# Kernel tuning notes

Hardware: AMD Instinct MI355X
Metric: run time of the kernel (lower is better)

The kernel has to match this reference:

```python
import jax, jax.numpy as jnp
import numpy as np

B, L, D_MODEL, D_K, HEADS, C = 4, 4096, 512, 64, 8, 2
TOPK = int(C * np.log(L))  # int(c * log(input_seq_len)) = 16


def setup_inputs() -> dict:
    key = jax.random.key(0)
    ks = jax.random.split(key, 5)
    q_in = jax.random.normal(ks[0], (B, L, D_MODEL), jnp.float32)
    k_in = jax.random.normal(ks[1], (B, L, D_MODEL), jnp.float32)
    v_in = jax.random.normal(ks[2], (B, L, D_MODEL), jnp.float32)
    Wq = jax.random.normal(ks[3], (D_MODEL, D_K), jnp.float32) / np.sqrt(D_MODEL)
    bq = jax.random.normal(ks[4], (D_K,), jnp.float32) * 0.01
    return {"q_in": q_in, "k_in": k_in, "v_in": v_in, "Wq": Wq, "bq": bq}


def _to_heads(x, Wq, bq):
    # Faithful to original: ALL of q/k/v use the `query` Dense layer, and all
    # heads are identical copies (same projection stacked `heads` times).
    p = x @ Wq + bq                       # [B, L, d_k]
    p = jnp.swapaxes(p, 1, 2)             # [B, d_k, L]  (transpose [0,3,2,1] of [B,L,d,H])
    return jnp.broadcast_to(p[:, None], (p.shape[0], HEADS, D_K, p.shape[-1]))  # [B,H,d,L]


def reference(q_in, k_in, v_in, Wq, bq):
    Q = jnp.fft.fft(_to_heads(q_in, Wq, bq).astype(jnp.complex64), axis=-1)
    K = jnp.fft.fft(_to_heads(k_in, Wq, bq).astype(jnp.complex64), axis=-1)
    V = _to_heads(v_in, Wq, bq)           # [B,H,d,L] float32
    QK = jnp.fft.ifft(Q * jnp.conj(K), axis=-1)   # circular cross-correlation
    qk_abs = jnp.abs(QK)                  # [B,H,d,L]

    vals, idx = jax.lax.top_k(qk_abs, TOPK)       # [B,H,d,k]
    w = jax.nn.softmax(vals, axis=-1)             # softmax over the k lags

    # tf.roll(v, shift=-lag): out[t] = v[(t + lag) mod L]  -> vectorized gather
    t = jnp.arange(L, dtype=jnp.int32)
    gidx = (idx[..., None] + t) % L               # [B,H,d,k,L]
    Vk = jnp.broadcast_to(V[:, :, :, None, :], gidx.shape)
    rolled = jnp.take_along_axis(Vk, gidx, axis=-1)           # [B,H,d,k,L]
    agg = jnp.sum(rolled * w[..., None], axis=3)              # [B,H,d,L]

    out = agg.reshape(agg.shape[0], HEADS * D_K, L)           # [B, H*d, L]
    return jnp.transpose(out, (0, 2, 1))                      # [B, L, H*d]
```

## Files before the change

### kernel.cpp

```cpp
#include <hip/hip_runtime.h>
#include <hip/hip_bf16.h>

#define BQ 4
#define LQ 4096
#define DM 512
#define DK 64
#define NROWS (BQ * DK)
#define TOPK 16
#define CAND 32

typedef __attribute__((ext_vector_type(4))) short short4v;
typedef __attribute__((ext_vector_type(8))) short short8v;
typedef __attribute__((ext_vector_type(16))) float f32x16;

__device__ __forceinline__ unsigned short f2bf(float x) {
  unsigned u = __builtin_bit_cast(unsigned, x);
  return (unsigned short)((u + 0x7FFFu + ((u >> 16) & 1u)) >> 16);
}
__device__ __forceinline__ float bf2f(unsigned short h) {
  unsigned u = ((unsigned)h) << 16;
  return __builtin_bit_cast(float, u);
}

__global__ __launch_bounds__(256) void proj_kernel(
    const float* __restrict__ q_in, const float* __restrict__ k_in,
    const float* __restrict__ v_in, const float* __restrict__ Wq,
    const float* __restrict__ bq, float* __restrict__ ws) {
  const float* x = blockIdx.z == 0 ? q_in : (blockIdx.z == 1 ? k_in : v_in);
  float* outp = ws + (size_t)blockIdx.z * (size_t)(NROWS * LQ);

  __shared__ __align__(16) short sm[27648];
  short* xh = sm;
  short* xl = sm + 9216;
  short* wh = sm + 18432;
  short* wl = sm + 23040;

  const int tid = threadIdx.x;
  const int l = tid & 63, wv = tid >> 6;
  const int R0 = blockIdx.x * 128;

  const int srow = tid >> 1;
  const int sp0 = (tid & 1) * 8;
  const int wcol = tid & 63;
  const int wk0 = (tid >> 6) * 16;

  f32x16 acc[2];
#pragma unroll
  for (int nt = 0; nt < 2; ++nt)
#pragma unroll
    for (int i = 0; i < 16; ++i) acc[nt][i] = 0.f;

  float4 xr[8];
  float wr[16];
#pragma unroll
  for (int c = 0; c < 8; ++c)
    xr[c] = *reinterpret_cast<const float4*>(
        &x[(size_t)(R0 + srow) * DM + (sp0 + c) * 4]);
#pragma unroll
  for (int u = 0; u < 16; ++u)
    wr[u] = Wq[(size_t)(wk0 + u) * DK + wcol];

  const int arow = wv * 32 + (l & 31);
  const int qn = l >> 5;
  const int aswz = 2 * ((arow >> 3) & 3);
  const int bc0 = l & 31;
  const int bswz0 = 2 * (((0 + bc0) >> 3) & 3);
  const int bswz1 = 2 * (((32 + bc0) >> 3) & 3);

  for (int kc = 0; kc < DM; kc += 64) {
    __syncthreads();
#pragma unroll
    for (int c = 0; c < 8; ++c) {
      int f4 = sp0 + c;
      int qd = (f4 >> 1) ^ (2 * ((srow >> 3) & 3));
      int base = srow * 72 + qd * 8 + (f4 & 1) * 4;
      float vv[4] = {xr[c].x, xr[c].y, xr[c].z, xr[c].w};
      short4v hi, lo;
#pragma unroll
      for (int i = 0; i < 4; ++i) {
        unsigned short h = f2bf(vv[i]);
        hi[i] = (short)h;
        lo[i] = (short)f2bf(vv[i] - bf2f(h));
      }
      *reinterpret_cast<short4v*>(xh + base) = hi;
      *reinterpret_cast<short4v*>(xl + base) = lo;
    }
#pragma unroll
    for (int qq = 0; qq < 2; ++qq) {
      int qd = ((wk0 >> 3) + qq) ^ (2 * ((wcol >> 3) & 3));
      int base = wcol * 72 + qd * 8;
      short8v hi, lo;
#pragma unroll
      for (int i = 0; i < 8; ++i) {
        float vv = wr[qq * 8 + i];
        unsigned short h = f2bf(vv);
        hi[i] = (short)h;
        lo[i] = (short)f2bf(vv - bf2f(h));
      }
      *reinterpret_cast<short8v*>(wh + base) = hi;
      *reinterpret_cast<short8v*>(wl + base) = lo;
    }
    __syncthreads();
    if (kc + 64 < DM) {
#pragma unroll
      for (int c = 0; c < 8; ++c)
        xr[c] = *reinterpret_cast<const float4*>(
            &x[(size_t)(R0 + srow) * DM + kc + 64 + (sp0 + c) * 4]);
#pragma unroll
      for (int u = 0; u < 16; ++u)
        wr[u] = Wq[(size_t)(kc + 64 + wk0 + u) * DK + wcol];
    }
#pragma unroll
    for (int ks = 0; ks < 4; ++ks) {
      int qA = (2 * ks + qn) ^ aswz;
      short8v ah = *reinterpret_cast<const short8v*>(xh + arow * 72 + qA * 8);
      short8v al_ = *reinterpret_cast<const short8v*>(xl + arow * 72 + qA * 8);
      {
        int qB = (2 * ks + qn) ^ bswz0;
        short8v bh = *reinterpret_cast<const short8v*>(wh + bc0 * 72 + qB * 8);
        short8v bl_ = *reinterpret_cast<const short8v*>(wl + bc0 * 72 + qB * 8);
        asm volatile("v_mfma_f32_32x32x16_bf16 %0, %1, %2, %0"
                     : "+v"(acc[0]) : "v"(ah), "v"(bh));
        asm volatile("v_mfma_f32_32x32x16_bf16 %0, %1, %2, %0"
                     : "+v"(acc[0]) : "v"(ah), "v"(bl_));
        asm volatile("v_mfma_f32_32x32x16_bf16 %0, %1, %2, %0"
                     : "+v"(acc[0]) : "v"(al_), "v"(bh));
      }
      {
        int qB = (2 * ks + qn) ^ bswz1;
        short8v bh = *reinterpret_cast<const short8v*>(wh + (32 + bc0) * 72 + qB * 8);
        short8v bl_ = *reinterpret_cast<const short8v*>(wl + (32 + bc0) * 72 + qB * 8);
        asm volatile("v_mfma_f32_32x32x16_bf16 %0, %1, %2, %0"
                     : "+v"(acc[1]) : "v"(ah), "v"(bh));
        asm volatile("v_mfma_f32_32x32x16_bf16 %0, %1, %2, %0"
                     : "+v"(acc[1]) : "v"(ah), "v"(bl_));
        asm volatile("v_mfma_f32_32x32x16_bf16 %0, %1, %2, %0"
                     : "+v"(acc[1]) : "v"(al_), "v"(bh));
      }
    }
  }

  asm volatile("s_nop 7\n\ts_nop 7\n\ts_nop 7" ::: "memory");
  __syncthreads();
  float* ts = (float*)sm;
  const int b = R0 >> 12, i0 = R0 & (LQ - 1);
  float bb[2] = {bq[l & 31], bq[32 + (l & 31)]};
#pragma unroll
  for (int nt = 0; nt < 2; ++nt) {
    float* area = ts + (wv * 2 + nt) * 1088;
#pragma unroll
    for (int r = 0; r < 16; ++r) {
      int io = (r & 3) + 8 * (r >> 2) + 4 * (l >> 5);
      area[(l & 31) * 34 + io] = acc[nt][r] + bb[nt];
    }
  }
  __syncthreads();
  const int e = l & 15, jg = l >> 4;
#pragma unroll
  for (int nt = 0; nt < 2; ++nt) {
    const float* area = ts + (wv * 2 + nt) * 1088;
#pragma unroll
    for (int p = 0; p < 8; ++p) {
      int jj = jg * 8 + p;
      float2 v = *reinterpret_cast<const float2*>(area + jj * 34 + e * 2);
      *reinterpret_cast<float2*>(
          &outp[((size_t)b * DK + nt * 32 + jj) * LQ + i0 + wv * 32 + e * 2]) = v;
    }
  }
}

__global__ __launch_bounds__(512) void corr_topk_kernel(
    const float* __restrict__ qp, const float* __restrict__ kp,
    float* __restrict__ lw) {
  const int row = blockIdx.x;
  const int tid = threadIdx.x;
  __shared__ __align__(16) short qs[3 * 4112 + 4096];
  __shared__ __align__(16) short ks[4096];
  __shared__ __align__(16) float qf[LQ];
  __shared__ __align__(16) float kf[LQ];
  __shared__ unsigned wk[128];
  __shared__ unsigned scand[CAND];
  __shared__ float rS[CAND];
  __shared__ float ordv[TOPK]; __shared__ int ordl[TOPK];

  const float* qr = qp + ((size_t)row << 12);
  const float* kr = kp + ((size_t)row << 12);

  {
    const float4* q4 = (const float4*)qr;
    float4 v0 = q4[tid * 2], v1 = q4[tid * 2 + 1];
    float4 v2 = q4[(tid * 2 + 2) & 1023];
    ((float4*)qf)[tid * 2] = v0;
    ((float4*)qf)[tid * 2 + 1] = v1;
    float f[12] = {v0.x, v0.y, v0.z, v0.w, v1.x, v1.y, v1.z, v1.w,
                   v2.x, v2.y, v2.z, v2.w};
#pragma unroll
    for (int r = 0; r < 4; ++r) {
      short8v o;
#pragma unroll
      for (int i = 0; i < 8; ++i) o[i] = (short)f2bf(f[i + r]);
      *(short8v*)(&qs[r * 4112 + tid * 8]) = o;
    }
    const float4* k4 = (const float4*)kr;
    float4 w0 = k4[tid * 2], w1 = k4[tid * 2 + 1];
    ((float4*)kf)[tid * 2] = w0;
    ((float4*)kf)[tid * 2 + 1] = w1;
    float g[8] = {w0.x, w0.y, w0.z, w0.w, w1.x, w1.y, w1.z, w1.w};
    int Q = tid;
    int Qs = Q ^ ((Q >> 3) & 7);
    short8v o;
#pragma unroll
    for (int i = 0; i < 8; ++i) o[i] = (short)f2bf(g[i]);
    *(short8v*)(&ks[Qs << 3]) = o;
  }
  __syncthreads();

  const int l = tid & 63, wv = tid >> 6;
  const int Oq = ((8 * (l >> 5) - 32 * (l & 31)) & 4095) >> 3;
  const int rB = (l & 31) & 3;
  const int Ce = (l & 31) + 8 * (l >> 5) - rB;
  const short* qb = qs + rB * 4112;

  f32x16 acc[4];
#pragma unroll
  for (int M = 0; M < 4; ++M)
#pragma unroll
    for (int i = 0; i < 16; ++i) acc[M][i] = 0.f;

  const int J0 = wv * 32;
#pragma unroll 2
  for (int jb = 0; jb < 32; ++jb) {
    const int J = J0 + jb;
    int e1 = (Ce + 16 * J) & 4095;
    int e2 = (e1 + 4) & 4095;
    uint2 blo = *(const uint2*)(qb + e1);
    uint2 bhi = *(const uint2*)(qb + e2);
    int4 bi; bi.x = blo.x; bi.y = blo.y; bi.z = bhi.x; bi.w = bhi.y;
    short8v bf = __builtin_bit_cast(short8v, bi);
    const int Dq = 2 * J;
#pragma unroll
    for (int M = 0; M < 4; ++M) {
      int Q = (Oq + Dq - 128 * M) & 511;
      Q ^= (Q >> 3) & 7;
      short8v af = *(const short8v*)(&ks[Q << 3]);
      asm volatile("v_mfma_f32_32x32x16_bf16 %0, %1, %2, %0"
                   : "+v"(acc[M]) : "v"(af), "v"(bf));
    }
  }

  asm volatile("s_nop 7\n\ts_nop 7\n\ts_nop 7" ::: "memory");
  __syncthreads();
  float* red = (float*)qs;
  const int strip = (wv & 1) * 4096;
  const int ch4 = (l >> 5) * 4, cn = l & 31;
#define RIDX(M, r) (strip + ((M) << 10) + 32 * (((r)&3) + 8 * ((r) >> 2) + ch4) + cn)
  if (wv < 2) {
#pragma unroll
    for (int M = 0; M < 4; ++M)
#pragma unroll
      for (int r = 0; r < 16; ++r) red[RIDX(M, r)] = acc[M][r];
  }
  __syncthreads();
  if (wv >= 2 && wv < 4) {
#pragma unroll
    for (int M = 0; M < 4; ++M)
#pragma unroll
      for (int r = 0; r < 16; ++r) red[RIDX(M, r)] += acc[M][r];
  }
  __syncthreads();
  if (wv >= 4 && wv < 6) {
#pragma unroll
    for (int M = 0; M < 4; ++M)
#pragma unroll
      for (int r = 0; r < 16; ++r) red[RIDX(M, r)] += acc[M][r];
  }
  __syncthreads();
  if (wv >= 6) {
#pragma unroll
    for (int M = 0; M < 4; ++M)
#pragma unroll
      for (int r = 0; r < 16; ++r) red[RIDX(M, r)] += acc[M][r];
  }
  __syncthreads();
#undef RIDX

  {
    unsigned key[8];
#pragma unroll
    for (int i = 0; i < 8; ++i) {
      int tau = wv * 512 + i * 64 + l;
      float v = red[tau] + red[4096 + tau];
      unsigned u = __builtin_bit_cast(unsigned, fabsf(v));
      key[i] = (u & 0xFFFFF000u) | (unsigned)(4095 - tau);
    }
    unsigned bkey = key[0];
#pragma unroll
    for (int i = 1; i < 8; ++i) bkey = key[i] > bkey ? key[i] : bkey;
    for (int round = 0; round < 16; ++round) {
      unsigned m = bkey;
#pragma unroll
      for (int off = 1; off < 64; off <<= 1) {
        unsigned o = __shfl_xor(m, off);
        m = o > m ? o : m;
      }
      if (l == 0) wk[wv * 16 + round] = m;
#pragma unroll
      for (int i = 0; i < 8; ++i) key[i] = (key[i] == m) ? 0u : key[i];
      bkey = key[0];
#pragma unroll
      for (int i = 1; i < 8; ++i) bkey = key[i] > bkey ? key[i] : bkey;
    }
  }
  __syncthreads();

  if (tid < 128) {
    unsigned ki = wk[tid];
    int rank = 0;
    for (int j = 0; j < 128; ++j) rank += (wk[j] > ki);
    if (rank < CAND) scand[rank] = ki;
  }
  __syncthreads();

  {
    const int ci = tid >> 4, sub = tid & 15;
    const int lag = 4095 - (int)(scand[ci] & 0xFFFu);
    float S0 = 0.f, S1 = 0.f, S2 = 0.f, S3 = 0.f;
    for (int it = 0; it < 256; it += 4) {
      int t0 = (it + 0) * 16 + sub, t1 = (it + 1) * 16 + sub;
      int t2 = (it + 2) * 16 + sub, t3 = (it + 3) * 16 + sub;
      S0 = fmaf(kf[t0], qf[(t0 + lag) & 4095], S0);
      S1 = fmaf(kf[t1], qf[(t1 + lag) & 4095], S1);
      S2 = fmaf(kf[t2], qf[(t2 + lag) & 4095], S2);
      S3 = fmaf(kf[t3], qf[(t3 + lag) & 4095], S3);
    }
    float S = (S0 + S1) + (S2 + S3);
    S += __shfl_xor(S, 1);
    S += __shfl_xor(S, 2);
    S += __shfl_xor(S, 4);
    S += __shfl_xor(S, 8);
    if (sub == 0) rS[ci] = S;
  }
  __syncthreads();

  if (tid < CAND) {
    float vi = fabsf(rS[tid]);
    int ii = 4095 - (int)(scand[tid] & 0xFFFu);
    int rank = 0;
    for (int j = 0; j < CAND; ++j) {
      float vj = fabsf(rS[j]);
      int ij = 4095 - (int)(scand[j] & 0xFFFu);
      rank += (vj > vi) || (vj == vi && ij < ii);
    }
    if (rank < TOPK) { ordv[rank] = vi; ordl[rank] = ii; }
  }
  __syncthreads();

  if (tid == 0) {
    float m0 = ordv[0], s = 0.f, e[TOPK];
    for (int k = 0; k < TOPK; ++k) { e[k] = expf(ordv[k] - m0); s += e[k]; }
    float inv = 1.f / s;
    int* ip = (int*)(lw + (size_t)row * 32);
    for (int k = 0; k < TOPK; ++k) {
      ip[k] = ordl[k];
      ((float*)ip)[TOPK + k] = e[k] * inv;
    }
  }
}

__global__ void agg_kernel(const float* __restrict__ vpT,
                           const float* __restrict__ lw,
                           float* __restrict__ aggT) {
  const int row = blockIdx.x, tid = threadIdx.x;
  __shared__ __align__(16) float vr[2 * LQ];
  __shared__ float w[TOPK]; __shared__ int lg[TOPK];

  const float* v0 = vpT + (size_t)row * LQ;
  for (int x = tid; x < LQ; x += 256) {
    float val = v0[x];
    vr[x] = val; vr[x + LQ] = val;
  }
  if (tid < TOPK) {
    lg[tid] = ((const int*)(lw + (size_t)row * 32))[tid];
    w[tid] = lw[(size_t)row * 32 + TOPK + tid];
  }
  __syncthreads();

  float wr[TOPK]; int lr[TOPK];
#pragma unroll
  for (int k = 0; k < TOPK; ++k) { wr[k] = w[k]; lr[k] = lg[k]; }

  for (int m = 0; m < 16; ++m) {
    int t = m * 256 + tid;
    float a = 0.f;
#pragma unroll
    for (int k = 0; k < TOPK; ++k) a = fmaf(wr[k], vr[t + lr[k]], a);
    aggT[(size_t)row * LQ + t] = a;
  }
}

__global__ void trans_kernel(const float* __restrict__ aggT,
                             float* __restrict__ out) {
  const int b = blockIdx.y;
  const int t0 = blockIdx.x * 64;
  const int tid = threadIdx.x;
  __shared__ float ts[64][65];

#pragma unroll
  for (int v = 0; v < 16; ++v) {
    int f = v * 256 + tid;
    int d = f >> 6, tt = f & 63;
    ts[d][tt] = aggT[((size_t)b * DK + d) * LQ + t0 + tt];
  }
  __syncthreads();

#pragma unroll
  for (int v = 0; v < 128; ++v) {
    int f = v * 256 + tid;
    int tt = f >> 9, c = f & 511;
    out[((size_t)b * LQ + t0 + tt) * (8 * DK) + c] = ts[c & 63][tt];
  }
}

extern "C" void kernel_launch(void* const* d_in, const int* in_sizes, int n_in,
                              void* d_out, int out_size, void* d_ws, size_t ws_size,
                              hipStream_t stream) {
  const float* q_in = (const float*)d_in[0];
  const float* k_in = (const float*)d_in[1];
  const float* v_in = (const float*)d_in[2];
  const float* Wq   = (const float*)d_in[3];
  const float* bq   = (const float*)d_in[4];
  float* out = (float*)d_out;
  float* ws  = (float*)d_ws;

  const size_t M = (size_t)NROWS * LQ;
  float* qp   = ws;
  float* kp   = ws + M;
  float* vp   = ws + 2 * M;
  float* lw   = ws + 3 * M;
  float* aggT = ws + 4 * M;

  proj_kernel<<<dim3(128, 1, 3), 256, 0, stream>>>(q_in, k_in, v_in, Wq, bq, ws);
  corr_topk_kernel<<<NROWS, 512, 0, stream>>>(qp, kp, lw);
  agg_kernel<<<NROWS, 256, 0, stream>>>(vp, lw, aggT);
  trans_kernel<<<dim3(LQ / 64, BQ), 256, 0, stream>>>(aggT, out);
}
```

Measured before the change: 76.48 us.

## Precompute split-bf16 transposed weights and stream projection operands directly into registers

A new small kernel converts Wq once per call into transposed bf16 hi/lo arrays in the workspace. The projection kernel then gives each wave its own 32 rows and loads the A fragments from global memory straight into registers, double-buffered, with B fragments read from the pre-split weights. This removes the LDS staging, the swizzling and the per-chunk __syncthreads. In exchange it adds an extra kernel launch and explicit s_nop padding around the MFMA instructions in both kernels, which may stall the instruction stream in the correlation kernel.

```diff
diff --git a/kernel.cpp b/kernel.cpp
--- a/kernel.cpp
+++ b/kernel.cpp
@@ -9,7 +9,6 @@
 #define TOPK 16
 #define CAND 32
 
-typedef __attribute__((ext_vector_type(4))) short short4v;
 typedef __attribute__((ext_vector_type(8))) short short8v;
 typedef __attribute__((ext_vector_type(16))) float f32x16;
 
@@ -22,27 +21,62 @@
   return __builtin_bit_cast(float, u);
 }
 
+__device__ __forceinline__ void mfma_drain() {
+  __builtin_amdgcn_sched_barrier(0);
+  asm volatile("s_nop 7\n\ts_nop 7\n\ts_nop 7\n\ts_nop 7" ::: "memory");
+  __builtin_amdgcn_sched_barrier(0);
+}
+
+__global__ __launch_bounds__(256) void wprep_kernel(
+    const float* __restrict__ Wq, short* __restrict__ whT,
+    short* __restrict__ wlT) {
+  __shared__ short lh[64][66];
+  __shared__ short ll[64][66];
+  const int tid = threadIdx.x;
+  const int k0 = blockIdx.x * 64;
+#pragma unroll
+  for (int p = 0; p < 16; ++p) {
+    int idx = p * 256 + tid;
+    int kr = idx >> 6, j = idx & 63;
+    float v = Wq[(size_t)(k0 + kr) * DK + j];
+    unsigned short h = f2bf(v);
+    lh[j][kr] = (short)h;
+    ll[j][kr] = (short)f2bf(v - bf2f(h));
+  }
+  __syncthreads();
+  const int j = tid >> 2, ks = (tid & 3) * 16;
+  short8v o0, o1;
+#pragma unroll
+  for (int i = 0; i < 8; ++i) { o0[i] = lh[j][ks + i]; o1[i] = lh[j][ks + 8 + i]; }
+  *(short8v*)(&whT[(size_t)j * DM + k0 + ks]) = o0;
+  *(short8v*)(&whT[(size_t)j * DM + k0 + ks + 8]) = o1;
+#pragma unroll
+  for (int i = 0; i < 8; ++i) { o0[i] = ll[j][ks + i]; o1[i] = ll[j][ks + 8 + i]; }
+  *(short8v*)(&wlT[(size_t)j * DM + k0 + ks]) = o0;
+  *(short8v*)(&wlT[(size_t)j * DM + k0 + ks + 8]) = o1;
+}
+
 __global__ __launch_bounds__(256) void proj_kernel(
     const float* __restrict__ q_in, const float* __restrict__ k_in,
-    const float* __restrict__ v_in, const float* __restrict__ Wq,
-    const float* __restrict__ bq, float* __restrict__ ws) {
+    const float* __restrict__ v_in, const short* __restrict__ whT,
+    const short* __restrict__ wlT, const float* __restrict__ bq,
+    float* __restrict__ ws) {
   const float* x = blockIdx.z == 0 ? q_in : (blockIdx.z == 1 ? k_in : v_in);
   float* outp = ws + (size_t)blockIdx.z * (size_t)(NROWS * LQ);
 
-  __shared__ __align__(16) short sm[27648];
-  short* xh = sm;
-  short* xl = sm + 9216;
-  short* wh = sm + 18432;
-  short* wl = sm + 23040;
+  __shared__ __align__(16) float ts[8 * 1088];
 
   const int tid = threadIdx.x;
   const int l = tid & 63, wv = tid >> 6;
-  const int R0 = blockIdx.x * 128;
-
-  const int srow = tid >> 1;
-  const int sp0 = (tid & 1) * 8;
-  const int wcol = tid & 63;
-  const int wk0 = (tid >> 6) * 16;
+  const int gw = blockIdx.x * 4 + wv;
+  const int R0 = gw * 32;
+  const int koff = 8 * (l >> 5);
+
+  const float* xb = x + (size_t)(R0 + (l & 31)) * DM + koff;
+  const short* bh0p = whT + (size_t)(l & 31) * DM + koff;
+  const short* bl0p = wlT + (size_t)(l & 31) * DM + koff;
+  const short* bh1p = whT + (size_t)(32 + (l & 31)) * DM + koff;
+  const short* bl1p = wlT + (size_t)(32 + (l & 31)) * DM + koff;
 
   f32x16 acc[2];
 #pragma unroll
@@ -50,99 +84,59 @@
 #pragma unroll
     for (int i = 0; i < 16; ++i) acc[nt][i] = 0.f;
 
-  float4 xr[8];
-  float wr[16];
-#pragma unroll
-  for (int c = 0; c < 8; ++c)
-    xr[c] = *reinterpret_cast<const float4*>(
-        &x[(size_t)(R0 + srow) * DM + (sp0 + c) * 4]);
-#pragma unroll
-  for (int u = 0; u < 16; ++u)
-    wr[u] = Wq[(size_t)(wk0 + u) * DK + wcol];
-
-  const int arow = wv * 32 + (l & 31);
-  const int qn = l >> 5;
-  const int aswz = 2 * ((arow >> 3) & 3);
-  const int bc0 = l & 31;
-  const int bswz0 = 2 * (((0 + bc0) >> 3) & 3);
-  const int bswz1 = 2 * (((32 + bc0) >> 3) & 3);
-
-  for (int kc = 0; kc < DM; kc += 64) {
-    __syncthreads();
-#pragma unroll
-    for (int c = 0; c < 8; ++c) {
-      int f4 = sp0 + c;
-      int qd = (f4 >> 1) ^ (2 * ((srow >> 3) & 3));
-      int base = srow * 72 + qd * 8 + (f4 & 1) * 4;
-      float vv[4] = {xr[c].x, xr[c].y, xr[c].z, xr[c].w};
-      short4v hi, lo;
-#pragma unroll
-      for (int i = 0; i < 4; ++i) {
-        unsigned short h = f2bf(vv[i]);
-        hi[i] = (short)h;
-        lo[i] = (short)f2bf(vv[i] - bf2f(h));
+  float4 a0[8], a1[8];
+#pragma unroll
+  for (int s = 0; s < 4; ++s) {
+    a0[2 * s]     = *(const float4*)(xb + s * 16);
+    a0[2 * s + 1] = *(const float4*)(xb + s * 16 + 4);
+  }
+
+#pragma unroll
+  for (int kb = 0; kb < 8; ++kb) {
+    if (kb < 7) {
+#pragma unroll
+      for (int s = 0; s < 4; ++s) {
+        a1[2 * s]     = *(const float4*)(xb + (kb + 1) * 64 + s * 16);
+        a1[2 * s + 1] = *(const float4*)(xb + (kb + 1) * 64 + s * 16 + 4);
       }
-      *reinterpret_cast<short4v*>(xh + base) = hi;
-      *reinterpret_cast<short4v*>(xl + base) = lo;
-    }
-#pragma unroll
-    for (int qq = 0; qq < 2; ++qq) {
-      int qd = ((wk0 >> 3) + qq) ^ (2 * ((wcol >> 3) & 3));
-      int base = wcol * 72 + qd * 8;
-      short8v hi, lo;
+    }
+#pragma unroll
+    for (int s = 0; s < 4; ++s) {
+      float f[8] = {a0[2 * s].x, a0[2 * s].y, a0[2 * s].z, a0[2 * s].w,
+                    a0[2 * s + 1].x, a0[2 * s + 1].y, a0[2 * s + 1].z,
+                    a0[2 * s + 1].w};
+      short8v ah, al;
 #pragma unroll
       for (int i = 0; i < 8; ++i) {
-        float vv = wr[qq * 8 + i];
-        unsigned short h = f2bf(vv);
-        hi[i] = (short)h;
-        lo[i] = (short)f2bf(vv - bf2f(h));
+        unsigned short h = f2bf(f[i]);
+        ah[i] = (short)h;
+        al[i] = (short)f2bf(f[i] - bf2f(h));
       }
-      *reinterpret_cast<short8v*>(wh + base) = hi;
-      *reinterpret_cast<short8v*>(wl + base) = lo;
-    }
-    __syncthreads();
-    if (kc + 64 < DM) {
-#pragma unroll
-      for (int c = 0; c < 8; ++c)
-        xr[c] = *reinterpret_cast<const float4*>(
-            &x[(size_t)(R0 + srow) * DM + kc + 64 + (sp0 + c) * 4]);
-#pragma unroll
-      for (int u = 0; u < 16; ++u)
-        wr[u] = Wq[(size_t)(kc + 64 + wk0 + u) * DK + wcol];
-    }
-#pragma unroll
-    for (int ks = 0; ks < 4; ++ks) {
-      int qA = (2 * ks + qn) ^ aswz;
-      short8v ah = *reinterpret_cast<const short8v*>(xh + arow * 72 + qA * 8);
-      short8v al_ = *reinterpret_cast<const short8v*>(xl + arow * 72 + qA * 8);
-      {
-        int qB = (2 * ks + qn) ^ bswz0;
-        short8v bh = *reinterpret_cast<const short8v*>(wh + bc0 * 72 + qB * 8);
-        short8v bl_ = *reinterpret_cast<const short8v*>(wl + bc0 * 72 + qB * 8);
-        asm volatile("v_mfma_f32_32x32x16_bf16 %0, %1, %2, %0"
-                     : "+v"(acc[0]) : "v"(ah), "v"(bh));
-        asm volatile("v_mfma_f32_32x32x16_bf16 %0, %1, %2, %0"
-                     : "+v"(acc[0]) : "v"(ah), "v"(bl_));
-        asm volatile("v_mfma_f32_32x32x16_bf16 %0, %1, %2, %0"
-                     : "+v"(acc[0]) : "v"(al_), "v"(bh));
-      }
-      {
-        int qB = (2 * ks + qn) ^ bswz1;
-        short8v bh = *reinterpret_cast<const short8v*>(wh + (32 + bc0) * 72 + qB * 8);
-        short8v bl_ = *reinterpret_cast<const short8v*>(wl + (32 + bc0) * 72 + qB * 8);
-        asm volatile("v_mfma_f32_32x32x16_bf16 %0, %1, %2, %0"
-                     : "+v"(acc[1]) : "v"(ah), "v"(bh));
-        asm volatile("v_mfma_f32_32x32x16_bf16 %0, %1, %2, %0"
-                     : "+v"(acc[1]) : "v"(ah), "v"(bl_));
-        asm volatile("v_mfma_f32_32x32x16_bf16 %0, %1, %2, %0"
-                     : "+v"(acc[1]) : "v"(al_), "v"(bh));
-      }
-    }
-  }
-
-  asm volatile("s_nop 7\n\ts_nop 7\n\ts_nop 7" ::: "memory");
-  __syncthreads();
-  float* ts = (float*)sm;
+      const int ko = kb * 64 + s * 16;
+      short8v bh0 = *(const short8v*)(bh0p + ko);
+      short8v bl0 = *(const short8v*)(bl0p + ko);
+      short8v bh1 = *(const short8v*)(bh1p + ko);
+      short8v bl1 = *(const short8v*)(bl1p + ko);
+      asm volatile(
+          "s_nop 4\n\t"
+          "v_mfma_f32_32x32x16_bf16 %0, %2, %4, %0\n\t"
+          "v_mfma_f32_32x32x16_bf16 %0, %2, %5, %0\n\t"
+          "v_mfma_f32_32x32x16_bf16 %0, %3, %4, %0\n\t"
+          "v_mfma_f32_32x32x16_bf16 %1, %2, %6, %1\n\t"
+          "v_mfma_f32_32x32x16_bf16 %1, %2, %7, %1\n\t"
+          "v_mfma_f32_32x32x16_bf16 %1, %3, %6, %1\n\t"
+          "s_nop 7\n\t"
+          "s_nop 3"
+          : "+v"(acc[0]), "+v"(acc[1])
+          : "v"(ah), "v"(al), "v"(bh0), "v"(bl0), "v"(bh1), "v"(bl1));
+    }
+    if (kb < 7) {
+#pragma unroll
+      for (int i = 0; i < 8; ++i) a0[i] = a1[i];
+    }
+  }
+
+  mfma_drain();
   const int b = R0 >> 12, i0 = R0 & (LQ - 1);
   float bb[2] = {bq[l & 31], bq[32 + (l & 31)]};
 #pragma unroll
@@ -164,7 +158,7 @@
       int jj = jg * 8 + p;
       float2 v = *reinterpret_cast<const float2*>(area + jj * 34 + e * 2);
       *reinterpret_cast<float2*>(
-          &outp[((size_t)b * DK + nt * 32 + jj) * LQ + i0 + wv * 32 + e * 2]) = v;
+          &outp[((size_t)b * DK + nt * 32 + jj) * LQ + i0 + e * 2]) = v;
     }
   }
 }
@@ -243,12 +237,15 @@
       int Q = (Oq + Dq - 128 * M) & 511;
       Q ^= (Q >> 3) & 7;
       short8v af = *(const short8v*)(&ks[Q << 3]);
-      asm volatile("v_mfma_f32_32x32x16_bf16 %0, %1, %2, %0"
+      asm volatile("s_nop 4\n\t"
+                   "v_mfma_f32_32x32x16_bf16 %0, %1, %2, %0\n\t"
+                   "s_nop 7\n\t"
+                   "s_nop 3"
                    : "+v"(acc[M]) : "v"(af), "v"(bf));
     }
   }
 
-  asm volatile("s_nop 7\n\ts_nop 7\n\ts_nop 7" ::: "memory");
+  mfma_drain();
   __syncthreads();
   float* red = (float*)qs;
   const int strip = (wv & 1) * 4096;
@@ -438,8 +435,12 @@
   float* vp   = ws + 2 * M;
   float* lw   = ws + 3 * M;
   float* aggT = ws + 4 * M;
-
-  proj_kernel<<<dim3(128, 1, 3), 256, 0, stream>>>(q_in, k_in, v_in, Wq, bq, ws);
+  short* whT  = (short*)(ws + 5 * M);
+  short* wlT  = (short*)(ws + 5 * M + 16384);
+
+  wprep_kernel<<<8, 256, 0, stream>>>(Wq, whT, wlT);
+  proj_kernel<<<dim3(128, 1, 3), 256, 0, stream>>>(q_in, k_in, v_in, whT, wlT,
+                                                   bq, ws);
   corr_topk_kernel<<<NROWS, 512, 0, stream>>>(qp, kp, lw);
   agg_kernel<<<NROWS, 256, 0, stream>>>(vp, lw, aggT);
   trans_kernel<<<dim3(LQ / 64, BQ), 256, 0, stream>>>(aggT, out);
```

After: 101.5 us. 1.33x slower.
